# Kernel optimization log

Hardware: AMD Instinct MI355X
Metric: run time of the kernel (lower is better)

The kernel has to match this reference:

```python
import jax, jax.numpy as jnp
import numpy as np

NEG_BIG = -10000000000.0  # value used by masked_fill_ in the original


def setup_inputs() -> dict:
    S, B, H = 2048, 16, 1024
    key = jax.random.key(0)
    ks = jax.random.split(key, 6)
    return {
        "hidden": jax.random.normal(ks[0], (1, B, H), dtype=jnp.float32),
        "hidden_sequence": jax.random.normal(ks[1], (S, B, H), dtype=jnp.float32),
        "input_masks": jax.random.randint(ks[2], (S, B), 0, 2) > 0,
        "W_att": jax.random.normal(ks[3], (H, 2 * H), dtype=jnp.float32) * (1.0 / np.sqrt(2 * H)),
        "b_att": jax.random.normal(ks[4], (H,), dtype=jnp.float32) * 0.01,
        "v": jax.random.normal(ks[5], (H,), dtype=jnp.float32),
    }


def reference(hidden, hidden_sequence, input_masks, W_att, b_att, v):
    S, B, H = hidden_sequence.shape
    # concat score: tanh(Linear([hidden; hidden_seq])) . v  -> [S, B]
    h = jnp.broadcast_to(hidden, (S, B, H))
    concat_hidden = jnp.concatenate([h, hidden_sequence], axis=2)  # [S, B, 2H]
    energy = jnp.tanh(jnp.einsum('sbk,hk->sbh', concat_hidden, W_att) + b_att)
    score = jnp.einsum('sbh,h->sb', energy, v)  # [S, B]
    # masked_fill_(~mask, -1e10); the original's .permute(1,0) result is discarded
    score = jnp.where(input_masks, score, jnp.float32(NEG_BIG))
    # faithful: softmax over dim=1 of the [S, B] energy (as in the source)
    attention_weight = jax.nn.softmax(score, axis=1)  # [S, B]
    # bmm([B,1,S], [B,S,H]) -> [B,1,H] -> permute(1,0,2) -> [1,B,H]
    context = jnp.einsum('sb,sbh->bh', attention_weight, hidden_sequence)[None, :, :]
    return context
```

## Files before the change

kernel.cpp:

```cpp
#include <hip/hip_runtime.h>
#include <math.h>

#define S_LEN 2048
#define B_SZ  16
#define H_SZ  1024
#define M_SZ  32768

typedef __attribute__((ext_vector_type(8))) _Float16 half8;
typedef __attribute__((ext_vector_type(4))) float f32x4;

__device__ __forceinline__ unsigned pack2h(float a, float b) {
    _Float16 ha = (_Float16)a, hb = (_Float16)b;
    unsigned short ua = __builtin_bit_cast(unsigned short, ha);
    unsigned short ub = __builtin_bit_cast(unsigned short, hb);
    return (unsigned)ua | ((unsigned)ub << 16);
}

__global__ __launch_bounds__(256)
void k_prep(const float* __restrict__ hidden,
            const float* __restrict__ W,
            const float* __restrict__ b_att,
            float* __restrict__ hp,
            unsigned short* __restrict__ Wh) {
    __shared__ float hid[B_SZ * H_SZ];
    const int t = threadIdx.x;
    #pragma unroll
    for (int i = 0; i < 16; ++i)
        *(float4*)&hid[(t + i * 256) * 4] = *(const float4*)(hidden + (t + i * 256) * 4);

    {
        const int r  = blockIdx.x * 4 + (t >> 6);
        const int c0 = (t & 63) * 16;
        const float* src = W + (size_t)r * 2048 + 1024 + c0;
        unsigned short* dst = Wh + (size_t)r * 1024 + c0;
        #pragma unroll
        for (int q = 0; q < 4; ++q) {
            float4 f = *(const float4*)(src + q * 4);
            uint2 u;
            u.x = pack2h(f.x, f.y);
            u.y = pack2h(f.z, f.w);
            *(uint2*)(dst + q * 4) = u;
        }
    }
    __syncthreads();

    const int lane = t & 63;
    const int h = blockIdx.x * 4 + (t >> 6);
    const float* w = W + (size_t)h * 2048;
    float acc[16];
    #pragma unroll
    for (int b = 0; b < 16; ++b) acc[b] = 0.f;
    for (int k = 0; k < H_SZ; k += 64) {
        float wv = w[k + lane];
        #pragma unroll
        for (int b = 0; b < 16; ++b) acc[b] = fmaf(wv, hid[b * H_SZ + k + lane], acc[b]);
    }
    #pragma unroll
    for (int b = 0; b < 16; ++b) {
        float s = acc[b];
        s += __shfl_xor(s, 1);  s += __shfl_xor(s, 2);  s += __shfl_xor(s, 4);
        s += __shfl_xor(s, 8);  s += __shfl_xor(s, 16); s += __shfl_xor(s, 32);
        if (lane == 0) hp[b * H_SZ + h] = s + b_att[h];
    }
}

#define SA    0
#define SB    8192
#define SBUF  16384

__global__ __launch_bounds__(256, 3)
void k_score_f16(const float* __restrict__ X,
                 const unsigned short* __restrict__ Wh,
                 const float* __restrict__ hp,
                 const float* __restrict__ v,
                 float* __restrict__ score_part) {
    __shared__ char lds[2 * SBUF];

    const int t = threadIdx.x;
    int wg = (blockIdx.x & 7) * 256 + (blockIdx.x >> 3);
    const int m0 = (wg >> 3) * 128;
    const int nt = wg & 7;
    const int n0 = nt * 128;

    const int lane = t & 63, wid = t >> 6;
    const int wm = wid >> 1, wn = wid & 1;
    const int lr = lane & 15, lq = lane >> 4;
    const int swr = (lq ^ ((lr >> 2) & 3)) * 16;

    const int srow = t >> 1, shalf = t & 1;
    const float* Xp = X + (size_t)(m0 + srow) * 1024 + shalf * 16;
    const unsigned short* Wp = Wh + (size_t)(n0 + srow) * 1024 + shalf * 16;
    const int sx = (srow >> 2) & 3;
    const int rowb = srow * 64;
    const int ws0 = rowb + ((shalf * 2 + 0) ^ sx) * 16;
    const int ws1 = rowb + ((shalf * 2 + 1) ^ sx) * 16;

    f32x4 acc[4][4];
    #pragma unroll
    for (int i = 0; i < 4; ++i)
        #pragma unroll
        for (int j = 0; j < 4; ++j) acc[i][j] = (f32x4)0.f;

    float4 ax[4];
    uint4 bx[2];

#define LOADG(kt)                                                              \
    {                                                                          \
        const int ko = (kt) * 32;                                              \
        ax[0] = *(const float4*)(Xp + ko);                                     \
        ax[1] = *(const float4*)(Xp + ko + 4);                                 \
        ax[2] = *(const float4*)(Xp + ko + 8);                                 \
        ax[3] = *(const float4*)(Xp + ko + 12);                                \
        bx[0] = *(const uint4*)(Wp + ko);                                      \
        bx[1] = *(const uint4*)(Wp + ko + 8);                                  \
    }

#define STAGE(buf)                                                             \
    {                                                                          \
        uint4 pa0, pa1;                                                        \
        pa0.x = pack2h(ax[0].x, ax[0].y); pa0.y = pack2h(ax[0].z, ax[0].w);    \
        pa0.z = pack2h(ax[1].x, ax[1].y); pa0.w = pack2h(ax[1].z, ax[1].w);    \
        pa1.x = pack2h(ax[2].x, ax[2].y); pa1.y = pack2h(ax[2].z, ax[2].w);    \
        pa1.z = pack2h(ax[3].x, ax[3].y); pa1.w = pack2h(ax[3].z, ax[3].w);    \
        *(uint4*)((buf) + SA + ws0) = pa0;                                     \
        *(uint4*)((buf) + SA + ws1) = pa1;                                     \
        *(uint4*)((buf) + SB + ws0) = bx[0];                                   \
        *(uint4*)((buf) + SB + ws1) = bx[1];                                   \
    }

    LOADG(0);
    STAGE(lds);
    __syncthreads();

    for (int kt = 0; kt < 32; ++kt) {
        char* cur = lds + (kt & 1) * SBUF;
        char* nxt = lds + ((kt & 1) ^ 1) * SBUF;
        if (kt < 31) LOADG(kt + 1);

        half8 ah[4], bh[4];
        #pragma unroll
        for (int i = 0; i < 4; ++i)
            ah[i] = *(const half8*)(cur + SA + (wm * 64 + i * 16 + lr) * 64 + swr);
        #pragma unroll
        for (int j = 0; j < 4; ++j)
            bh[j] = *(const half8*)(cur + SB + (wn * 64 + j * 16 + lr) * 64 + swr);

        #pragma unroll
        for (int i = 0; i < 4; ++i)
            #pragma unroll
            for (int j = 0; j < 4; ++j)
                acc[i][j] = __builtin_amdgcn_mfma_f32_16x16x32_f16(ah[i], bh[j], acc[i][j], 0, 0, 0);

        if (kt < 31) STAGE(nxt);
        __syncthreads();
    }

    float* red = (float*)lds;
    #pragma unroll
    for (int i = 0; i < 4; ++i) {
        #pragma unroll
        for (int r = 0; r < 4; ++r) {
            const int b = lq * 4 + r;
            float s = 0.f;
            #pragma unroll
            for (int j = 0; j < 4; ++j) {
                const int c = n0 + wn * 64 + j * 16 + lr;
                s += v[c] * tanhf(acc[i][j][r] + hp[b * H_SZ + c]);
            }
            s += __shfl_xor(s, 1);
            s += __shfl_xor(s, 2);
            s += __shfl_xor(s, 4);
            s += __shfl_xor(s, 8);
            if (lr == 0)
                red[wn * 128 + wm * 64 + i * 16 + lq * 4 + r] = s;
        }
    }
    __syncthreads();
    if (t < 128)
        score_part[nt * M_SZ + m0 + t] = red[t] + red[128 + t];
#undef LOADG
#undef STAGE
}

__global__ __launch_bounds__(256)
void k_context_sm(const float* __restrict__ part,
                  const int* __restrict__ masks,
                  const float* __restrict__ X,
                  float* __restrict__ partial) {
    __shared__ float wlds[64];

    const int t = threadIdx.x;
    const int b = blockIdx.x & 15;
    const int c = blockIdx.x >> 4;

    if (t < 64) {
        const int s = c * 64 + t;
        float vals[16];
        float mx = -INFINITY;
        #pragma unroll
        for (int bb = 0; bb < 16; ++bb) {
            const int m = s * 16 + bb;
            float sc = 0.f;
            #pragma unroll
            for (int p = 0; p < 8; ++p) sc += part[p * M_SZ + m];
            sc = masks[m] ? sc : -1e10f;
            vals[bb] = sc;
            mx = fmaxf(mx, sc);
        }
        float sum = 0.f;
        #pragma unroll
        for (int bb = 0; bb < 16; ++bb) { vals[bb] = __expf(vals[bb] - mx); sum += vals[bb]; }
        wlds[t] = vals[b] / sum;
    }
    __syncthreads();

    const int h = t * 4;
    float4 acc = make_float4(0.f, 0.f, 0.f, 0.f);
    #pragma unroll 4
    for (int i = 0; i < 64; ++i) {
        float w = wlds[i];
        float4 x = *(const float4*)(X + ((size_t)((c * 64 + i) * 16 + b)) * 1024 + h);
        acc.x += w * x.x; acc.y += w * x.y; acc.z += w * x.z; acc.w += w * x.w;
    }
    *(float4*)(partial + (size_t)(c * 16 + b) * 1024 + h) = acc;
}

__global__ void k_context_reduce(const float* __restrict__ partial,
                                 float* __restrict__ out) {
    int o = blockIdx.x * blockDim.x + threadIdx.x;
    int b = o >> 10, h = o & 1023;
    float s = 0.f;
    #pragma unroll
    for (int cc = 0; cc < 32; ++cc) s += partial[(size_t)(cc * 16 + b) * 1024 + h];
    out[o] = s;
}

extern "C" void kernel_launch(void* const* d_in, const int* in_sizes, int n_in,
                              void* d_out, int out_size, void* d_ws, size_t ws_size,
                              hipStream_t stream) {
    const float* hidden = (const float*)d_in[0];
    const float* hseq   = (const float*)d_in[1];
    const int*   masks  = (const int*)d_in[2];
    const float* W      = (const float*)d_in[3];
    const float* b_att  = (const float*)d_in[4];
    const float* v      = (const float*)d_in[5];
    float* out = (float*)d_out;

    float* wsf        = (float*)d_ws;
    float* hp         = wsf;
    float* score_part = wsf + 16384;
    float* partial    = score_part + 8 * M_SZ;
    unsigned short* Wh = (unsigned short*)(partial + 32 * 16 * 1024);

    hipLaunchKernelGGL(k_prep,           dim3(256),  dim3(256), 0, stream, hidden, W, b_att, hp, Wh);
    hipLaunchKernelGGL(k_score_f16,      dim3(2048), dim3(256), 0, stream, hseq, Wh, hp, v, score_part);
    hipLaunchKernelGGL(k_context_sm,     dim3(512),  dim3(256), 0, stream, score_part, masks, hseq, partial);
    hipLaunchKernelGGL(k_context_reduce, dim3(64),   dim3(256), 0, stream, partial, out);
}
```

Baseline: 371.7 us.

## Pre-swizzle fp16 W tiles and stream them into LDS with global_load_lds DMA

Rewrites the W conversion to emit fp16 weights already arranged in the swizzled per-tile LDS layout, so the score GEMM can copy B tiles straight into shared memory with global_load_lds instead of going through registers. The A operand (hidden_sequence) is still loaded into registers, converted and stored, using a new XOR swizzle shared with the B layout. The old fused prep kernel is split into a separate hidden-projection kernel (one wave per (b,h) dot product) and a conversion kernel, which adds a launch. Correctness relies on the DMA writes completing before the barrier, since no explicit vmcnt wait is visible.

```diff
diff --git a/kernel.cpp b/kernel.cpp
--- a/kernel.cpp
+++ b/kernel.cpp
@@ -16,52 +16,46 @@
     return (unsigned)ua | ((unsigned)ub << 16);
 }
 
-__global__ __launch_bounds__(256)
-void k_prep(const float* __restrict__ hidden,
-            const float* __restrict__ W,
-            const float* __restrict__ b_att,
-            float* __restrict__ hp,
-            unsigned short* __restrict__ Wh) {
-    __shared__ float hid[B_SZ * H_SZ];
-    const int t = threadIdx.x;
-    #pragma unroll
-    for (int i = 0; i < 16; ++i)
-        *(float4*)&hid[(t + i * 256) * 4] = *(const float4*)(hidden + (t + i * 256) * 4);
-
-    {
-        const int r  = blockIdx.x * 4 + (t >> 6);
-        const int c0 = (t & 63) * 16;
-        const float* src = W + (size_t)r * 2048 + 1024 + c0;
-        unsigned short* dst = Wh + (size_t)r * 1024 + c0;
-        #pragma unroll
-        for (int q = 0; q < 4; ++q) {
-            float4 f = *(const float4*)(src + q * 4);
-            uint2 u;
-            u.x = pack2h(f.x, f.y);
-            u.y = pack2h(f.z, f.w);
-            *(uint2*)(dst + q * 4) = u;
-        }
-    }
-    __syncthreads();
-
-    const int lane = t & 63;
-    const int h = blockIdx.x * 4 + (t >> 6);
-    const float* w = W + (size_t)h * 2048;
-    float acc[16];
-    #pragma unroll
-    for (int b = 0; b < 16; ++b) acc[b] = 0.f;
-    for (int k = 0; k < H_SZ; k += 64) {
-        float wv = w[k + lane];
-        #pragma unroll
-        for (int b = 0; b < 16; ++b) acc[b] = fmaf(wv, hid[b * H_SZ + k + lane], acc[b]);
-    }
-    #pragma unroll
-    for (int b = 0; b < 16; ++b) {
-        float s = acc[b];
-        s += __shfl_xor(s, 1);  s += __shfl_xor(s, 2);  s += __shfl_xor(s, 4);
-        s += __shfl_xor(s, 8);  s += __shfl_xor(s, 16); s += __shfl_xor(s, 32);
-        if (lane == 0) hp[b * H_SZ + h] = s + b_att[h];
-    }
+__device__ __forceinline__ int phys_off(int r, int sl) {
+    return ((r >> 1) << 7) + ((((r & 1) << 2 | sl) ^ ((r >> 1) & 7)) << 4);
+}
+
+__device__ __forceinline__ void dma16(const void* g, void* l) {
+    __builtin_amdgcn_global_load_lds(
+        (const __attribute__((address_space(1))) unsigned int*)g,
+        (__attribute__((address_space(3))) unsigned int*)l, 16, 0, 0);
+}
+
+__global__ void k_hidden_part(const float* __restrict__ hidden,
+                              const float* __restrict__ W,
+                              const float* __restrict__ b_att,
+                              float* __restrict__ hp) {
+    int gid  = blockIdx.x * blockDim.x + threadIdx.x;
+    int wave = gid >> 6;
+    int lane = threadIdx.x & 63;
+    int b = wave >> 10;
+    int h = wave & 1023;
+    const float* x = hidden + b * H_SZ;
+    const float* w = W + (size_t)h * (2 * H_SZ);
+    float acc = 0.f;
+    #pragma unroll
+    for (int k = 0; k < H_SZ; k += 64) acc += x[k + lane] * w[k + lane];
+    #pragma unroll
+    for (int off = 32; off; off >>= 1) acc += __shfl_down(acc, off, 64);
+    if (lane == 0) hp[b * H_SZ + h] = acc + b_att[h];
+}
+
+__global__ void k_convw(const float* __restrict__ W,
+                        unsigned short* __restrict__ Wsw) {
+    int t = blockIdx.x * 256 + threadIdx.x;
+    int sl = t & 3, r = (t >> 2) & 127, kt = (t >> 9) & 31, nt = t >> 14;
+    const float* src = W + (size_t)(nt * 128 + r) * 2048 + 1024 + kt * 32 + sl * 8;
+    float4 f0 = *(const float4*)src;
+    float4 f1 = *(const float4*)(src + 4);
+    uint4 u;
+    u.x = pack2h(f0.x, f0.y); u.y = pack2h(f0.z, f0.w);
+    u.z = pack2h(f1.x, f1.y); u.w = pack2h(f1.z, f1.w);
+    *(uint4*)((char*)Wsw + (size_t)(nt * 32 + kt) * 8192 + phys_off(r, sl)) = u;
 }
 
 #define SA    0
@@ -69,8 +63,8 @@
 #define SBUF  16384
 
 __global__ __launch_bounds__(256, 3)
-void k_score_f16(const float* __restrict__ X,
-                 const unsigned short* __restrict__ Wh,
+void k_score_dma(const float* __restrict__ X,
+                 const unsigned short* __restrict__ Wsw,
                  const float* __restrict__ hp,
                  const float* __restrict__ v,
                  float* __restrict__ score_part) {
@@ -85,15 +79,20 @@
     const int lane = t & 63, wid = t >> 6;
     const int wm = wid >> 1, wn = wid & 1;
     const int lr = lane & 15, lq = lane >> 4;
-    const int swr = (lq ^ ((lr >> 2) & 3)) * 16;
 
     const int srow = t >> 1, shalf = t & 1;
     const float* Xp = X + (size_t)(m0 + srow) * 1024 + shalf * 16;
-    const unsigned short* Wp = Wh + (size_t)(n0 + srow) * 1024 + shalf * 16;
-    const int sx = (srow >> 2) & 3;
-    const int rowb = srow * 64;
-    const int ws0 = rowb + ((shalf * 2 + 0) ^ sx) * 16;
-    const int ws1 = rowb + ((shalf * 2 + 1) ^ sx) * 16;
+    const int aOff0 = phys_off(srow, shalf * 2 + 0);
+    const int aOff1 = phys_off(srow, shalf * 2 + 1);
+
+    const unsigned short* Bp = Wsw + (size_t)(nt * 32) * 4096 + wid * 1024 + lane * 8;
+
+    int aro[4], bro[4];
+    #pragma unroll
+    for (int i = 0; i < 4; ++i) {
+        aro[i] = phys_off(wm * 64 + i * 16 + lr, lq);
+        bro[i] = phys_off(wn * 64 + i * 16 + lr, lq);
+    }
 
     f32x4 acc[4][4];
     #pragma unroll
@@ -102,48 +101,52 @@
         for (int j = 0; j < 4; ++j) acc[i][j] = (f32x4)0.f;
 
     float4 ax[4];
-    uint4 bx[2];
-
-#define LOADG(kt)                                                              \
+
+#define LOADA(kt)                                                              \
     {                                                                          \
-        const int ko = (kt) * 32;                                              \
-        ax[0] = *(const float4*)(Xp + ko);                                     \
-        ax[1] = *(const float4*)(Xp + ko + 4);                                 \
-        ax[2] = *(const float4*)(Xp + ko + 8);                                 \
-        ax[3] = *(const float4*)(Xp + ko + 12);                                \
-        bx[0] = *(const uint4*)(Wp + ko);                                      \
-        bx[1] = *(const uint4*)(Wp + ko + 8);                                  \
-    }
-
-#define STAGE(buf)                                                             \
+        const float* p = Xp + (kt) * 32;                                       \
+        ax[0] = *(const float4*)(p);                                           \
+        ax[1] = *(const float4*)(p + 4);                                       \
+        ax[2] = *(const float4*)(p + 8);                                       \
+        ax[3] = *(const float4*)(p + 12);                                      \
+    }
+
+#define DMAB(bufbase, kt)                                                      \
     {                                                                          \
-        uint4 pa0, pa1;                                                        \
-        pa0.x = pack2h(ax[0].x, ax[0].y); pa0.y = pack2h(ax[0].z, ax[0].w);    \
-        pa0.z = pack2h(ax[1].x, ax[1].y); pa0.w = pack2h(ax[1].z, ax[1].w);    \
-        pa1.x = pack2h(ax[2].x, ax[2].y); pa1.y = pack2h(ax[2].z, ax[2].w);    \
-        pa1.z = pack2h(ax[3].x, ax[3].y); pa1.w = pack2h(ax[3].z, ax[3].w);    \
-        *(uint4*)((buf) + SA + ws0) = pa0;                                     \
-        *(uint4*)((buf) + SA + ws1) = pa1;                                     \
-        *(uint4*)((buf) + SB + ws0) = bx[0];                                   \
-        *(uint4*)((buf) + SB + ws1) = bx[1];                                   \
-    }
-
-    LOADG(0);
-    STAGE(lds);
+        const unsigned short* s0 = Bp + (size_t)(kt) * 4096;                   \
+        dma16(s0,       (bufbase) + SB + wid * 2048);                          \
+        dma16(s0 + 512, (bufbase) + SB + wid * 2048 + 1024);                   \
+    }
+
+#define STAGEA(bufbase)                                                        \
+    {                                                                          \
+        uint4 p0, p1;                                                          \
+        p0.x = pack2h(ax[0].x, ax[0].y); p0.y = pack2h(ax[0].z, ax[0].w);      \
+        p0.z = pack2h(ax[1].x, ax[1].y); p0.w = pack2h(ax[1].z, ax[1].w);      \
+        p1.x = pack2h(ax[2].x, ax[2].y); p1.y = pack2h(ax[2].z, ax[2].w);      \
+        p1.z = pack2h(ax[3].x, ax[3].y); p1.w = pack2h(ax[3].z, ax[3].w);      \
+        *(uint4*)((bufbase) + SA + aOff0) = p0;                                \
+        *(uint4*)((bufbase) + SA + aOff1) = p1;                                \
+    }
+
+    LOADA(0);
+    DMAB(lds, 0);
+    STAGEA(lds);
     __syncthreads();
 
     for (int kt = 0; kt < 32; ++kt) {
         char* cur = lds + (kt & 1) * SBUF;
         char* nxt = lds + ((kt & 1) ^ 1) * SBUF;
-        if (kt < 31) LOADG(kt + 1);
+        if (kt < 31) {
+            LOADA(kt + 1);
+            DMAB(nxt, kt + 1);
+        }
 
         half8 ah[4], bh[4];
         #pragma unroll
-        for (int i = 0; i < 4; ++i)
-            ah[i] = *(const half8*)(cur + SA + (wm * 64 + i * 16 + lr) * 64 + swr);
-        #pragma unroll
-        for (int j = 0; j < 4; ++j)
-            bh[j] = *(const half8*)(cur + SB + (wn * 64 + j * 16 + lr) * 64 + swr);
+        for (int i = 0; i < 4; ++i) ah[i] = *(const half8*)(cur + SA + aro[i]);
+        #pragma unroll
+        for (int j = 0; j < 4; ++j) bh[j] = *(const half8*)(cur + SB + bro[j]);
 
         #pragma unroll
         for (int i = 0; i < 4; ++i)
@@ -151,7 +154,7 @@
             for (int j = 0; j < 4; ++j)
                 acc[i][j] = __builtin_amdgcn_mfma_f32_16x16x32_f16(ah[i], bh[j], acc[i][j], 0, 0, 0);
 
-        if (kt < 31) STAGE(nxt);
+        if (kt < 31) STAGEA(nxt);
         __syncthreads();
     }
 
@@ -178,8 +181,9 @@
     __syncthreads();
     if (t < 128)
         score_part[nt * M_SZ + m0 + t] = red[t] + red[128 + t];
-#undef LOADG
-#undef STAGE
+#undef LOADA
+#undef DMAB
+#undef STAGEA
 }
 
 __global__ __launch_bounds__(256)
@@ -250,10 +254,11 @@
     float* hp         = wsf;
     float* score_part = wsf + 16384;
     float* partial    = score_part + 8 * M_SZ;
-    unsigned short* Wh = (unsigned short*)(partial + 32 * 16 * 1024);
-
-    hipLaunchKernelGGL(k_prep,           dim3(256),  dim3(256), 0, stream, hidden, W, b_att, hp, Wh);
-    hipLaunchKernelGGL(k_score_f16,      dim3(2048), dim3(256), 0, stream, hseq, Wh, hp, v, score_part);
+    unsigned short* Wsw = (unsigned short*)(partial + 32 * 16 * 1024);
+
+    hipLaunchKernelGGL(k_hidden_part,    dim3(4096), dim3(256), 0, stream, hidden, W, b_att, hp);
+    hipLaunchKernelGGL(k_convw,          dim3(512),  dim3(256), 0, stream, W, Wsw);
+    hipLaunchKernelGGL(k_score_dma,      dim3(2048), dim3(256), 0, stream, hseq, Wsw, hp, v, score_part);
     hipLaunchKernelGGL(k_context_sm,     dim3(512),  dim3(256), 0, stream, score_part, masks, hseq, partial);
     hipLaunchKernelGGL(k_context_reduce, dim3(64),   dim3(256), 0, stream, partial, out);
 }
```

New measurement: 382.8 us. +3.0%, slower.
